# Optimization experiments

Measured on AMD Instinct MI355X. Metric: run time of the kernel, lower is better.

The kernel has to match this reference:

```python
import jax, jax.numpy as jnp
import numpy as np

DT = 0.01
V_REST = 0.0


def setup_inputs() -> dict:
    key = jax.random.key(0)
    ks = jax.random.split(key, 9)
    S, N, T = 64, 128, 1000
    w = jax.random.normal(ks[0], (N, N), dtype=jnp.float32) / jnp.sqrt(jnp.float32(N))
    ic = jax.random.uniform(ks[1], (N,), dtype=jnp.float32)
    v0 = jax.random.uniform(ks[2], (S, N), dtype=jnp.float32)
    i0 = jax.random.uniform(ks[3], (S, N), dtype=jnp.float32)
    # spike-clock state starts at minus an Exponential(1) draw; event fires when it hits 0
    u0 = jax.random.uniform(ks[4], (S, N), dtype=jnp.float32, minval=1e-6, maxval=1.0)
    s0 = jnp.log(u0)
    mu = jax.random.uniform(ks[5], (2,), dtype=jnp.float32, minval=0.5, maxval=1.0)
    sg = jax.random.normal(ks[6], (2, 2), dtype=jnp.float32)
    sigma = 0.1 * jnp.dot(sg, sg.T)  # PSD diffusion matrix as in __init__
    noise = jax.random.normal(ks[7], (T, S, N, 2), dtype=jnp.float32)
    ue = jax.random.uniform(ks[8], (T, S, N), dtype=jnp.float32, minval=1e-6, maxval=1.0)
    exp_draws = -jnp.log(ue)
    return {"w": w, "ic": ic, "v0": v0, "i0": i0, "s0": s0,
            "mu": mu, "sigma": sigma, "noise": noise, "exp_draws": exp_draws}


def reference(w, ic, v0, i0, s0, mu, sigma, noise, exp_draws):
    """Euler-Maruyama integration of the spiking-neuron jump-SDE.

    Per neuron state y = (v, i, s):
      dv = mu1*(i + ic - v) dt + (sigma dW)_0
      di = -mu2*i dt        + (sigma dW)_1
      ds = intensity_fn(v) dt   (intensity_fn = softplus)
    Spike event when s crosses 0 (cond_fn = y[:, 2]):
      v -> v_rest, postsynaptic currents i += spikes @ w, s -> -Exp(1) redraw.
    Returns ys of shape (samples, neurons, times, 3).
    """
    mu1, mu2 = mu[0], mu[1]
    dW = noise * jnp.sqrt(jnp.asarray(DT, noise.dtype))  # [T,S,N,2]

    def step(carry, xs):
        v, i, s = carry
        dw, edraw = xs
        # drift
        dv = mu1 * (i + ic - v)
        di = -mu2 * i
        ds = jax.nn.softplus(v)  # intensity_fn
        # diffusion on (v,i) channels: sigma @ dW per neuron
        nvi = jnp.einsum('snk,jk->snj', dw, sigma)  # [S,N,2]
        v = v + DT * dv + nvi[..., 0]
        i = i + DT * di + nvi[..., 1]
        s = s + DT * ds
        spike = s >= 0.0  # event detection (cond_fn hits zero)
        spk = spike.astype(v.dtype)
        i = i + spk @ w                    # network coupling jump
        v = jnp.where(spike, V_REST, v)    # membrane reset
        s = jnp.where(spike, -edraw, s)    # redraw exponential spike clock
        return (v, i, s), jnp.stack([v, i, s], axis=-1)  # [S,N,3]

    (_, _, _), ys = jax.lax.scan(step, (v0, i0, s0), (dW, exp_draws))
    # ys: [T,S,N,3] -> [S,N,T,3] (samples, neurons, times, 3)
    return jnp.transpose(ys, (1, 2, 0, 3))
```

## Files before the change

kernel.cpp:

```cpp
#include <hip/hip_runtime.h>
#include <cmath>

#define NS 64
#define NN 128
#define NT 1000
#define CH 8
#define WROWS 130
#define WL_DW (WROWS * NN)
#define OBUF_DW (2 * CH * 3 * NN)
#define LDS_BYTES ((WL_DW + OBUF_DW) * 4 + 32)

__device__ __forceinline__ float softplus_np(float x) {
    float r = fmaxf(x, 0.0f) + log1pf(expf(-fabsf(x)));
    return (x == 0.0f) ? 0.693147180559945309f : r;
}

__device__ __forceinline__ void sync_lds() {
    __builtin_amdgcn_sched_barrier(0);
    asm volatile("s_waitcnt lgkmcnt(0)" ::: "memory");
    __builtin_amdgcn_s_barrier();
    __builtin_amdgcn_sched_barrier(0);
}

__global__ __launch_bounds__(192) void snn_scan_kernel(
    const float* __restrict__ w,
    const float* __restrict__ ic,
    const float* __restrict__ v0,
    const float* __restrict__ i0,
    const float* __restrict__ s0,
    const float* __restrict__ mu,
    const float* __restrict__ sigma,
    const float* __restrict__ noise,
    const float* __restrict__ exp_draws,
    float* __restrict__ out)
{
    #pragma clang fp contract(off)
    extern __shared__ float smem[];
    float* wl   = smem;
    float* obuf = smem + WL_DW;
    unsigned long long* mslot =
        (unsigned long long*)(smem + WL_DW + OBUF_DW);

    const int samp = blockIdx.x;
    const int tid  = threadIdx.x;
    const int wid  = tid >> 6;
    const int l    = tid & 63;
    const int n    = (wid << 6) | l;

    if (tid < 128) {
        const float4* src = (const float4*)w;
        float4* dst = (float4*)wl;
        #pragma unroll
        for (int it = 0; it < 32; ++it)
            dst[it * 128 + tid] = src[it * 128 + tid];
        ((float2*)(wl + NN * NN))[tid] = make_float2(0.0f, 0.0f);
    }

    const float SQDT  = sqrtf(0.01f);
    const float DTf   = 0.01f;
    const float LOGE2 = 0.693147180559945309f;

    float* outb = out + (size_t)samp * NN * NT * 3;

    float mu1 = 0.f, negmu2 = 0.f, g00 = 0.f, g01 = 0.f, g10 = 0.f, g11 = 0.f;
    float icn = 0.f, v_ = 0.f, i_ = 0.f, s_ = 0.f, sp = 0.f;
    float2 nb0 = {}, nb1 = {}, nb2 = {}, nb3 = {}, nb4 = {}, nb5 = {}, nb6 = {}, nb7 = {};
    float  eb0 = 0, eb1 = 0, eb2 = 0, eb3 = 0, eb4 = 0, eb5 = 0, eb6 = 0, eb7 = 0;

    const float* nzb = noise + (size_t)samp * (NN * 2) + n * 2;
    const float* edb = exp_draws + (size_t)samp * NN + n;

    if (wid < 2) {
        __builtin_amdgcn_s_setprio(1);
        mu1 = mu[0]; negmu2 = -mu[1];
        g00 = sigma[0]; g01 = sigma[1]; g10 = sigma[2]; g11 = sigma[3];
        icn = ic[n];
        v_ = v0[samp * NN + n];
        i_ = i0[samp * NN + n];
        s_ = s0[samp * NN + n];
        sp = softplus_np(v_);
        nb0 = *(const float2*)(nzb + 0ull * (NS * NN * 2)); eb0 = edb[0ull * (NS * NN)];
        nb1 = *(const float2*)(nzb + 1ull * (NS * NN * 2)); eb1 = edb[1ull * (NS * NN)];
        nb2 = *(const float2*)(nzb + 2ull * (NS * NN * 2)); eb2 = edb[2ull * (NS * NN)];
        nb3 = *(const float2*)(nzb + 3ull * (NS * NN * 2)); eb3 = edb[3ull * (NS * NN)];
        nb4 = *(const float2*)(nzb + 4ull * (NS * NN * 2)); eb4 = edb[4ull * (NS * NN)];
        nb5 = *(const float2*)(nzb + 5ull * (NS * NN * 2)); eb5 = edb[5ull * (NS * NN)];
        nb6 = *(const float2*)(nzb + 6ull * (NS * NN * 2)); eb6 = edb[6ull * (NS * NN)];
        nb7 = *(const float2*)(nzb + 7ull * (NS * NN * 2)); eb7 = edb[7ull * (NS * NN)];
    }
    sync_lds();

    if (wid < 2) {
        int cur = 0;
        float* ob = obuf + n;

        auto STEP = [&](int k, int blk, float2& nb, float& eb) {
            #pragma clang fp contract(off)
            const int t = blk * CH + k;
            s_ = s_ + DTf * sp;
            const bool kk = (s_ >= 0.0f);
            const unsigned long long mym = __ballot(kk);
            if (l == 0) mslot[(k & 1) * 2 + wid] = mym;
            sync_lds();
            const float2 nz = nb;
            const float  ed = eb;
            const int tp = (t + 8) < NT ? (t + 8) : NT - 1;
            nb = *(const float2*)(nzb + (size_t)tp * (NS * NN * 2));
            eb = edb[(size_t)tp * (NS * NN)];

            const float dw0 = nz.x * SQDT, dw1 = nz.y * SQDT;
            const float nv = (dw0 * g00) + (dw1 * g01);
            const float ni = (dw0 * g10) + (dw1 * g11);
            const float tt = (i_ + icn) - v_;
            const float vt = (v_ + DTf * (mu1 * tt)) + nv;
            const float it = (i_ + DTf * (negmu2 * i_)) + ni;
            const float spv = softplus_np(vt);

            unsigned long long m0 = mslot[(k & 1) * 2 + 0];
            unsigned long long m1 = mslot[(k & 1) * 2 + 1];

            float a = 0.0f;
            if (m0 | m1) {
                auto ext1 = [&]() -> int {
                    const bool u0 = (m0 != 0);
                    const unsigned long long m = u0 ? m0 : m1;
                    const int b = m ? (int)__builtin_ctzll(m) : 99;
                    const int r = (b == 99) ? 128 : ((u0 ? 0 : 64) + b);
                    const unsigned long long m0n = m0 & (m0 - 1);
                    const unsigned long long m1n = m1 & (m1 - 1);
                    m0 = u0 ? m0n : m0;
                    m1 = u0 ? m1 : m1n;
                    return r;
                };
                const int r1 = ext1(); const int r2 = ext1();
                const int r3 = ext1(); const int r4 = ext1();
                const float q1 = wl[r1 * NN + n];
                const float q2 = wl[r2 * NN + n];
                const float q3 = wl[r3 * NN + n];
                const float q4 = wl[r4 * NN + n];
                a = q1;  a += q2;  a += q3;  a += q4;
                #pragma clang loop unroll(disable)
                while (m0 | m1) {
                    const int r = ext1();
                    a += wl[r * NN + n];
                }
            }
            i_ = it + a;

            v_ = kk ? 0.0f : vt;
            s_ = kk ? -ed : s_;
            sp = kk ? LOGE2 : spv;

            float* row = ob + (cur * CH * 3 + k * 3) * NN;
            row[0 * NN] = v_;
            row[1 * NN] = i_;
            row[2 * NN] = s_;
        };

        #pragma clang loop unroll(disable)
        for (int blk = 0; blk < NT / CH; ++blk) {
            STEP(0, blk, nb0, eb0);
            STEP(1, blk, nb1, eb1);
            STEP(2, blk, nb2, eb2);
            STEP(3, blk, nb3, eb3);
            STEP(4, blk, nb4, eb4);
            STEP(5, blk, nb5, eb5);
            STEP(6, blk, nb6, eb6);
            STEP(7, blk, nb7, eb7);
            cur ^= 1;
        }
    } else {
        auto flush3 = [&](int b, int tb0, int kk) {
            const float* ob2 = obuf + b * (CH * 3 * NN);
            #pragma unroll
            for (int j = 3 * kk; j < 3 * kk + 3; ++j) {
                const int f = j * 64 + l;
                const int nn2 = f / 12;
                const int da = 2 * (f - nn2 * 12);
                const float x = ob2[(da    ) * NN + nn2];
                const float y = ob2[(da + 1) * NN + nn2];
                *(float2*)(outb + (size_t)nn2 * (NT * 3) + (size_t)tb0 * 3 + da) =
                    make_float2(x, y);
            }
        };
        int cur = 0;
        #pragma clang loop unroll(disable)
        for (int blk = 0; blk < NT / CH; ++blk) {
            #pragma clang loop unroll(disable)
            for (int k = 0; k < CH; ++k) {
                sync_lds();
                if (blk > 0) flush3(cur ^ 1, (blk - 1) * CH, k);
            }
            cur ^= 1;
        }
    }

    sync_lds();

    if (wid == 2) {
        const float* ob2 = obuf + 0 * (CH * 3 * NN);
        #pragma unroll
        for (int j = 0; j < 24; ++j) {
            const int f = j * 64 + l;
            const int nn2 = f / 12;
            const int da = 2 * (f - nn2 * 12);
            const float x = ob2[(da    ) * NN + nn2];
            const float y = ob2[(da + 1) * NN + nn2];
            *(float2*)(outb + (size_t)nn2 * (NT * 3) + (size_t)(NT - CH) * 3 + da) =
                make_float2(x, y);
        }
    }
}

extern "C" void kernel_launch(void* const* d_in, const int* in_sizes, int n_in,
                              void* d_out, int out_size, void* d_ws, size_t ws_size,
                              hipStream_t stream) {
    const float* w         = (const float*)d_in[0];
    const float* ic        = (const float*)d_in[1];
    const float* v0        = (const float*)d_in[2];
    const float* i0        = (const float*)d_in[3];
    const float* s0        = (const float*)d_in[4];
    const float* mu        = (const float*)d_in[5];
    const float* sigma     = (const float*)d_in[6];
    const float* noise     = (const float*)d_in[7];
    const float* exp_draws = (const float*)d_in[8];
    float* out = (float*)d_out;

    (void)hipFuncSetAttribute((const void*)snn_scan_kernel,
                              hipFuncAttributeMaxDynamicSharedMemorySize,
                              LDS_BYTES);

    snn_scan_kernel<<<dim3(NS), dim3(192), LDS_BYTES, stream>>>(
        w, ic, v0, i0, s0, mu, sigma, noise, exp_draws, out);
}
```

Before: 575.4 us.

## Redundantly track mirror wave's spike clock to move barrier off critical path

Each compute wave now also integrates the spike clock of its partner neuron (n^64), so it can build both halves of the spike mask locally with two ballots instead of exchanging masks through LDS before the coupling step. The partner's softplus intensity is passed through a small LDS buffer after a barrier at the end of each step, one step delayed. This moves the barrier from the start of the step to the end, so the dependency chain into the weight-row gather is shorter. The output staging buffer is also padded to stride 129 to reduce bank conflicts. The cost is extra exp_draws loads, extra registers, and duplicated clock arithmetic.

```diff
diff --git a/kernel.cpp b/kernel.cpp
--- a/kernel.cpp
+++ b/kernel.cpp
@@ -5,10 +5,13 @@
 #define NN 128
 #define NT 1000
 #define CH 8
+#define NNP 129
 #define WROWS 130
 #define WL_DW (WROWS * NN)
-#define OBUF_DW (2 * CH * 3 * NN)
-#define LDS_BYTES ((WL_DW + OBUF_DW) * 4 + 32)
+#define OB_HALF (3 * CH * NNP)
+#define OBUF_DW (2 * OB_HALF)
+#define SPV_DW (2 * NN)
+#define LDS_BYTES ((WL_DW + OBUF_DW + SPV_DW) * 4)
 
 __device__ __forceinline__ float softplus_np(float x) {
     float r = fmaxf(x, 0.0f) + log1pf(expf(-fabsf(x)));
@@ -36,16 +39,16 @@
 {
     #pragma clang fp contract(off)
     extern __shared__ float smem[];
-    float* wl   = smem;
-    float* obuf = smem + WL_DW;
-    unsigned long long* mslot =
-        (unsigned long long*)(smem + WL_DW + OBUF_DW);
+    float* wl     = smem;
+    float* obuf   = smem + WL_DW;
+    float* spvbuf = smem + WL_DW + OBUF_DW;
 
     const int samp = blockIdx.x;
     const int tid  = threadIdx.x;
     const int wid  = tid >> 6;
     const int l    = tid & 63;
     const int n    = (wid << 6) | l;
+    const int nm   = n ^ 64;
 
     if (tid < 128) {
         const float4* src = (const float4*)w;
@@ -64,11 +67,15 @@
 
     float mu1 = 0.f, negmu2 = 0.f, g00 = 0.f, g01 = 0.f, g10 = 0.f, g11 = 0.f;
     float icn = 0.f, v_ = 0.f, i_ = 0.f, s_ = 0.f, sp = 0.f;
+    float s_m = 0.f, spvm_pend = 0.f;
+    bool  km_prev = false;
     float2 nb0 = {}, nb1 = {}, nb2 = {}, nb3 = {}, nb4 = {}, nb5 = {}, nb6 = {}, nb7 = {};
-    float  eb0 = 0, eb1 = 0, eb2 = 0, eb3 = 0, eb4 = 0, eb5 = 0, eb6 = 0, eb7 = 0;
+    float  eo0 = 0, eo1 = 0, eo2 = 0, eo3 = 0, eo4 = 0, eo5 = 0, eo6 = 0, eo7 = 0;
+    float  em0 = 0, em1 = 0, em2 = 0, em3 = 0, em4 = 0, em5 = 0, em6 = 0, em7 = 0;
 
     const float* nzb = noise + (size_t)samp * (NN * 2) + n * 2;
-    const float* edb = exp_draws + (size_t)samp * NN + n;
+    const float* edo = exp_draws + (size_t)samp * NN + n;
+    const float* edm = exp_draws + (size_t)samp * NN + nm;
 
     if (wid < 2) {
         __builtin_amdgcn_s_setprio(1);
@@ -79,35 +86,32 @@
         i_ = i0[samp * NN + n];
         s_ = s0[samp * NN + n];
         sp = softplus_np(v_);
-        nb0 = *(const float2*)(nzb + 0ull * (NS * NN * 2)); eb0 = edb[0ull * (NS * NN)];
-        nb1 = *(const float2*)(nzb + 1ull * (NS * NN * 2)); eb1 = edb[1ull * (NS * NN)];
-        nb2 = *(const float2*)(nzb + 2ull * (NS * NN * 2)); eb2 = edb[2ull * (NS * NN)];
-        nb3 = *(const float2*)(nzb + 3ull * (NS * NN * 2)); eb3 = edb[3ull * (NS * NN)];
-        nb4 = *(const float2*)(nzb + 4ull * (NS * NN * 2)); eb4 = edb[4ull * (NS * NN)];
-        nb5 = *(const float2*)(nzb + 5ull * (NS * NN * 2)); eb5 = edb[5ull * (NS * NN)];
-        nb6 = *(const float2*)(nzb + 6ull * (NS * NN * 2)); eb6 = edb[6ull * (NS * NN)];
-        nb7 = *(const float2*)(nzb + 7ull * (NS * NN * 2)); eb7 = edb[7ull * (NS * NN)];
+        s_m = s0[samp * NN + nm];
+        spvm_pend = softplus_np(v0[samp * NN + nm]);
+        nb0 = *(const float2*)(nzb + 0ull * (NS * NN * 2)); eo0 = edo[0ull * (NS * NN)]; em0 = edm[0ull * (NS * NN)];
+        nb1 = *(const float2*)(nzb + 1ull * (NS * NN * 2)); eo1 = edo[1ull * (NS * NN)]; em1 = edm[1ull * (NS * NN)];
+        nb2 = *(const float2*)(nzb + 2ull * (NS * NN * 2)); eo2 = edo[2ull * (NS * NN)]; em2 = edm[2ull * (NS * NN)];
+        nb3 = *(const float2*)(nzb + 3ull * (NS * NN * 2)); eo3 = edo[3ull * (NS * NN)]; em3 = edm[3ull * (NS * NN)];
+        nb4 = *(const float2*)(nzb + 4ull * (NS * NN * 2)); eo4 = edo[4ull * (NS * NN)]; em4 = edm[4ull * (NS * NN)];
+        nb5 = *(const float2*)(nzb + 5ull * (NS * NN * 2)); eo5 = edo[5ull * (NS * NN)]; em5 = edm[5ull * (NS * NN)];
+        nb6 = *(const float2*)(nzb + 6ull * (NS * NN * 2)); eo6 = edo[6ull * (NS * NN)]; em6 = edm[6ull * (NS * NN)];
+        nb7 = *(const float2*)(nzb + 7ull * (NS * NN * 2)); eo7 = edo[7ull * (NS * NN)]; em7 = edm[7ull * (NS * NN)];
     }
     sync_lds();
 
     if (wid < 2) {
-        int cur = 0;
-        float* ob = obuf + n;
-
-        auto STEP = [&](int k, int blk, float2& nb, float& eb) {
+        auto STEP = [&](int k, int blk, float2& nb, float& eo, float& em) {
             #pragma clang fp contract(off)
             const int t = blk * CH + k;
+            const int par = k & 1;
             s_ = s_ + DTf * sp;
             const bool kk = (s_ >= 0.0f);
-            const unsigned long long mym = __ballot(kk);
-            if (l == 0) mslot[(k & 1) * 2 + wid] = mym;
-            sync_lds();
-            const float2 nz = nb;
-            const float  ed = eb;
-            const int tp = (t + 8) < NT ? (t + 8) : NT - 1;
+            const unsigned long long mown = __ballot(kk);
+            const float2 nz = nb; const float edv = eo; const float edmv = em;
+            const int tp = (t + CH) < NT ? (t + CH) : NT - 1;
             nb = *(const float2*)(nzb + (size_t)tp * (NS * NN * 2));
-            eb = edb[(size_t)tp * (NS * NN)];
-
+            eo = edo[(size_t)tp * (NS * NN)];
+            em = edm[(size_t)tp * (NS * NN)];
             const float dw0 = nz.x * SQDT, dw1 = nz.y * SQDT;
             const float nv = (dw0 * g00) + (dw1 * g01);
             const float ni = (dw0 * g10) + (dw1 * g11);
@@ -115,10 +119,13 @@
             const float vt = (v_ + DTf * (mu1 * tt)) + nv;
             const float it = (i_ + DTf * (negmu2 * i_)) + ni;
             const float spv = softplus_np(vt);
-
-            unsigned long long m0 = mslot[(k & 1) * 2 + 0];
-            unsigned long long m1 = mslot[(k & 1) * 2 + 1];
-
+            spvbuf[par * NN + n] = spv;
+            const float spm = km_prev ? LOGE2 : spvm_pend;
+            s_m = s_m + DTf * spm;
+            const bool kmir = (s_m >= 0.0f);
+            const unsigned long long mmir = __ballot(kmir);
+            unsigned long long m0 = (wid == 0) ? mown : mmir;
+            unsigned long long m1 = (wid == 0) ? mmir : mown;
             float a = 0.0f;
             if (m0 | m1) {
                 auto ext1 = [&]() -> int {
@@ -146,66 +153,64 @@
                 }
             }
             i_ = it + a;
-
             v_ = kk ? 0.0f : vt;
-            s_ = kk ? -ed : s_;
+            s_ = kk ? -edv : s_;
             sp = kk ? LOGE2 : spv;
-
-            float* row = ob + (cur * CH * 3 + k * 3) * NN;
-            row[0 * NN] = v_;
-            row[1 * NN] = i_;
-            row[2 * NN] = s_;
+            s_m = kmir ? -edmv : s_m;
+            float* row = obuf + (blk & 1) * OB_HALF + (k * 3) * NNP + n;
+            row[0 * NNP] = v_;
+            row[1 * NNP] = i_;
+            row[2 * NNP] = s_;
+            sync_lds();
+            spvm_pend = spvbuf[par * NN + nm];
+            km_prev = kmir;
         };
 
         #pragma clang loop unroll(disable)
         for (int blk = 0; blk < NT / CH; ++blk) {
-            STEP(0, blk, nb0, eb0);
-            STEP(1, blk, nb1, eb1);
-            STEP(2, blk, nb2, eb2);
-            STEP(3, blk, nb3, eb3);
-            STEP(4, blk, nb4, eb4);
-            STEP(5, blk, nb5, eb5);
-            STEP(6, blk, nb6, eb6);
-            STEP(7, blk, nb7, eb7);
-            cur ^= 1;
+            STEP(0, blk, nb0, eo0, em0);
+            STEP(1, blk, nb1, eo1, em1);
+            STEP(2, blk, nb2, eo2, em2);
+            STEP(3, blk, nb3, eo3, em3);
+            STEP(4, blk, nb4, eo4, em4);
+            STEP(5, blk, nb5, eo5, em5);
+            STEP(6, blk, nb6, eo6, em6);
+            STEP(7, blk, nb7, eo7, em7);
         }
     } else {
-        auto flush3 = [&](int b, int tb0, int kk) {
-            const float* ob2 = obuf + b * (CH * 3 * NN);
+        auto flush3 = [&](int h, int tb0, int kk) {
+            const float* ob2 = obuf + h * OB_HALF;
             #pragma unroll
             for (int j = 3 * kk; j < 3 * kk + 3; ++j) {
                 const int f = j * 64 + l;
                 const int nn2 = f / 12;
                 const int da = 2 * (f - nn2 * 12);
-                const float x = ob2[(da    ) * NN + nn2];
-                const float y = ob2[(da + 1) * NN + nn2];
+                const float x = ob2[(da    ) * NNP + nn2];
+                const float y = ob2[(da + 1) * NNP + nn2];
                 *(float2*)(outb + (size_t)nn2 * (NT * 3) + (size_t)tb0 * 3 + da) =
                     make_float2(x, y);
             }
         };
-        int cur = 0;
         #pragma clang loop unroll(disable)
         for (int blk = 0; blk < NT / CH; ++blk) {
             #pragma clang loop unroll(disable)
             for (int k = 0; k < CH; ++k) {
                 sync_lds();
-                if (blk > 0) flush3(cur ^ 1, (blk - 1) * CH, k);
+                if (blk > 0) flush3((blk - 1) & 1, (blk - 1) * CH, k);
             }
-            cur ^= 1;
         }
     }
 
     sync_lds();
-
     if (wid == 2) {
-        const float* ob2 = obuf + 0 * (CH * 3 * NN);
+        const float* ob2 = obuf + ((NT / CH - 1) & 1) * OB_HALF;
         #pragma unroll
         for (int j = 0; j < 24; ++j) {
             const int f = j * 64 + l;
             const int nn2 = f / 12;
             const int da = 2 * (f - nn2 * 12);
-            const float x = ob2[(da    ) * NN + nn2];
-            const float y = ob2[(da + 1) * NN + nn2];
+            const float x = ob2[(da    ) * NNP + nn2];
+            const float y = ob2[(da + 1) * NNP + nn2];
             *(float2*)(outb + (size_t)nn2 * (NT * 3) + (size_t)(NT - CH) * 3 + da) =
                 make_float2(x, y);
         }
```

Result: no change. 583.9 us (+1.5%).

## Pack two samples per block sharing weight LDS, pad output buffer

Applied to the files above, without the earlier changes.

Each block now handles two samples with 384 threads (3 waves per sample), sharing one LDS copy of the weight matrix, and launches half as many blocks. The output staging buffer is padded to 129 columns to reduce LDS bank conflicts on the transposing flush, the sched_barriers and setprio are removed, and the unrolled spike gather is cut from 4 to 2 rows. The aim is to reduce per-block weight loading, improve the LDS read pattern, and shorten the common spike path. The cost is that both samples now synchronise on shared block-wide barriers, so each step waits on the slower of the two samples, and only 32 blocks run on a large GPU.

```diff
diff --git a/kernel.cpp b/kernel.cpp
--- a/kernel.cpp
+++ b/kernel.cpp
@@ -5,10 +5,13 @@
 #define NN 128
 #define NT 1000
 #define CH 8
+#define NNP 129
 #define WROWS 130
 #define WL_DW (WROWS * NN)
-#define OBUF_DW (2 * CH * 3 * NN)
-#define LDS_BYTES ((WL_DW + OBUF_DW) * 4 + 32)
+#define OB_HALF (3 * CH * NNP)
+#define OBUF_PS (2 * OB_HALF)
+#define MS_DW 8
+#define LDS_BYTES ((WL_DW + 2 * OBUF_PS + 2 * MS_DW) * 4)
 
 __device__ __forceinline__ float softplus_np(float x) {
     float r = fmaxf(x, 0.0f) + log1pf(expf(-fabsf(x)));
@@ -16,13 +19,12 @@
 }
 
 __device__ __forceinline__ void sync_lds() {
-    __builtin_amdgcn_sched_barrier(0);
     asm volatile("s_waitcnt lgkmcnt(0)" ::: "memory");
     __builtin_amdgcn_s_barrier();
-    __builtin_amdgcn_sched_barrier(0);
-}
-
-__global__ __launch_bounds__(192) void snn_scan_kernel(
+    asm volatile("" ::: "memory");
+}
+
+__global__ __launch_bounds__(384) void snn_scan_kernel(
     const float* __restrict__ w,
     const float* __restrict__ ic,
     const float* __restrict__ v0,
@@ -36,16 +38,19 @@
 {
     #pragma clang fp contract(off)
     extern __shared__ float smem[];
-    float* wl   = smem;
-    float* obuf = smem + WL_DW;
+    float* wl = smem;
+
+    const int tid = threadIdx.x;
+    const int wid = tid >> 6;
+    const int ss  = (wid >= 3) ? 1 : 0;
+    const int wr  = wid - 3 * ss;
+    const int l   = tid & 63;
+    const int samp = blockIdx.x * 2 + ss;
+    const int n    = (wr << 6) | l;
+
+    float* obuf = smem + WL_DW + ss * OBUF_PS;
     unsigned long long* mslot =
-        (unsigned long long*)(smem + WL_DW + OBUF_DW);
-
-    const int samp = blockIdx.x;
-    const int tid  = threadIdx.x;
-    const int wid  = tid >> 6;
-    const int l    = tid & 63;
-    const int n    = (wid << 6) | l;
+        (unsigned long long*)(smem + WL_DW + 2 * OBUF_PS) + ss * 4;
 
     if (tid < 128) {
         const float4* src = (const float4*)w;
@@ -70,8 +75,7 @@
     const float* nzb = noise + (size_t)samp * (NN * 2) + n * 2;
     const float* edb = exp_draws + (size_t)samp * NN + n;
 
-    if (wid < 2) {
-        __builtin_amdgcn_s_setprio(1);
+    if (wr < 2) {
         mu1 = mu[0]; negmu2 = -mu[1];
         g00 = sigma[0]; g01 = sigma[1]; g10 = sigma[2]; g11 = sigma[3];
         icn = ic[n];
@@ -90,21 +94,18 @@
     }
     sync_lds();
 
-    if (wid < 2) {
-        int cur = 0;
-        float* ob = obuf + n;
-
+    if (wr < 2) {
         auto STEP = [&](int k, int blk, float2& nb, float& eb) {
             #pragma clang fp contract(off)
             const int t = blk * CH + k;
             s_ = s_ + DTf * sp;
             const bool kk = (s_ >= 0.0f);
             const unsigned long long mym = __ballot(kk);
-            if (l == 0) mslot[(k & 1) * 2 + wid] = mym;
+            if (l == 0) mslot[(k & 1) * 2 + wr] = mym;
             sync_lds();
             const float2 nz = nb;
             const float  ed = eb;
-            const int tp = (t + 8) < NT ? (t + 8) : NT - 1;
+            const int tp = (t + CH) < NT ? (t + CH) : NT - 1;
             nb = *(const float2*)(nzb + (size_t)tp * (NS * NN * 2));
             eb = edb[(size_t)tp * (NS * NN)];
 
@@ -133,12 +134,9 @@
                     return r;
                 };
                 const int r1 = ext1(); const int r2 = ext1();
-                const int r3 = ext1(); const int r4 = ext1();
                 const float q1 = wl[r1 * NN + n];
                 const float q2 = wl[r2 * NN + n];
-                const float q3 = wl[r3 * NN + n];
-                const float q4 = wl[r4 * NN + n];
-                a = q1;  a += q2;  a += q3;  a += q4;
+                a = q1;  a += q2;
                 #pragma clang loop unroll(disable)
                 while (m0 | m1) {
                     const int r = ext1();
@@ -151,10 +149,10 @@
             s_ = kk ? -ed : s_;
             sp = kk ? LOGE2 : spv;
 
-            float* row = ob + (cur * CH * 3 + k * 3) * NN;
-            row[0 * NN] = v_;
-            row[1 * NN] = i_;
-            row[2 * NN] = s_;
+            float* row = obuf + (blk & 1) * OB_HALF + (k * 3) * NNP + n;
+            row[0 * NNP] = v_;
+            row[1 * NNP] = i_;
+            row[2 * NNP] = s_;
         };
 
         #pragma clang loop unroll(disable)
@@ -167,45 +165,41 @@
             STEP(5, blk, nb5, eb5);
             STEP(6, blk, nb6, eb6);
             STEP(7, blk, nb7, eb7);
-            cur ^= 1;
         }
     } else {
-        auto flush3 = [&](int b, int tb0, int kk) {
-            const float* ob2 = obuf + b * (CH * 3 * NN);
+        auto flush3 = [&](int h, int tb0, int kk) {
+            const float* ob2 = obuf + h * OB_HALF;
             #pragma unroll
             for (int j = 3 * kk; j < 3 * kk + 3; ++j) {
                 const int f = j * 64 + l;
                 const int nn2 = f / 12;
                 const int da = 2 * (f - nn2 * 12);
-                const float x = ob2[(da    ) * NN + nn2];
-                const float y = ob2[(da + 1) * NN + nn2];
+                const float x = ob2[(da    ) * NNP + nn2];
+                const float y = ob2[(da + 1) * NNP + nn2];
                 *(float2*)(outb + (size_t)nn2 * (NT * 3) + (size_t)tb0 * 3 + da) =
                     make_float2(x, y);
             }
         };
-        int cur = 0;
         #pragma clang loop unroll(disable)
         for (int blk = 0; blk < NT / CH; ++blk) {
             #pragma clang loop unroll(disable)
             for (int k = 0; k < CH; ++k) {
                 sync_lds();
-                if (blk > 0) flush3(cur ^ 1, (blk - 1) * CH, k);
+                if (blk > 0) flush3((blk - 1) & 1, (blk - 1) * CH, k);
             }
-            cur ^= 1;
         }
     }
 
     sync_lds();
-
-    if (wid == 2) {
-        const float* ob2 = obuf + 0 * (CH * 3 * NN);
+    if (wr == 2) {
+        const float* ob2 = obuf + ((NT / CH - 1) & 1) * OB_HALF;
         #pragma unroll
         for (int j = 0; j < 24; ++j) {
             const int f = j * 64 + l;
             const int nn2 = f / 12;
             const int da = 2 * (f - nn2 * 12);
-            const float x = ob2[(da    ) * NN + nn2];
-            const float y = ob2[(da + 1) * NN + nn2];
+            const float x = ob2[(da    ) * NNP + nn2];
+            const float y = ob2[(da + 1) * NNP + nn2];
             *(float2*)(outb + (size_t)nn2 * (NT * 3) + (size_t)(NT - CH) * 3 + da) =
                 make_float2(x, y);
         }
@@ -230,6 +224,6 @@
                               hipFuncAttributeMaxDynamicSharedMemorySize,
                               LDS_BYTES);
 
-    snn_scan_kernel<<<dim3(NS), dim3(192), LDS_BYTES, stream>>>(
+    snn_scan_kernel<<<dim3(NS / 2), dim3(384), LDS_BYTES, stream>>>(
         w, ic, v0, i0, s0, mu, sigma, noise, exp_draws, out);
 }
```

After: 715.8 us. +24.4%, slower.

## Compute all 128 neurons in one wavefront to remove per-step barriers

Applied to the files above, without the earlier changes.

The scan now runs in a single wave, with each lane handling two neurons as float2 pairs. Spike masks come from two ballots inside the wave, so the per-timestep LDS mask exchange and block barrier go away, leaving one barrier per 8-step chunk. The weight matrix is re-laid out as interleaved pairs, and the output staging buffer is padded to avoid bank conflicts. The trade-off is less parallelism on the serial critical path: each lane now does twice the softplus and gather work, and a single writer wave flushes a whole chunk at a time.

```diff
diff --git a/kernel.cpp b/kernel.cpp
--- a/kernel.cpp
+++ b/kernel.cpp
@@ -5,10 +5,15 @@
 #define NN 128
 #define NT 1000
 #define CH 8
+#define OBP 65
 #define WROWS 130
-#define WL_DW (WROWS * NN)
-#define OBUF_DW (2 * CH * 3 * NN)
-#define LDS_BYTES ((WL_DW + OBUF_DW) * 4 + 32)
+#define WP_F2 (WROWS * 64)
+#define WL_DW (WP_F2 * 2)
+#define OB_HALF_F2 (CH * 3 * OBP)
+#define OBUF_DW (2 * OB_HALF_F2 * 2)
+#define LDS_BYTES ((WL_DW + OBUF_DW) * 4)
+
+typedef float f2 __attribute__((ext_vector_type(2)));
 
 __device__ __forceinline__ float softplus_np(float x) {
     float r = fmaxf(x, 0.0f) + log1pf(expf(-fabsf(x)));
@@ -16,13 +21,12 @@
 }
 
 __device__ __forceinline__ void sync_lds() {
-    __builtin_amdgcn_sched_barrier(0);
     asm volatile("s_waitcnt lgkmcnt(0)" ::: "memory");
     __builtin_amdgcn_s_barrier();
-    __builtin_amdgcn_sched_barrier(0);
-}
-
-__global__ __launch_bounds__(192) void snn_scan_kernel(
+    asm volatile("" ::: "memory");
+}
+
+__global__ __launch_bounds__(128) void snn_scan_kernel(
     const float* __restrict__ w,
     const float* __restrict__ ic,
     const float* __restrict__ v0,
@@ -36,179 +40,166 @@
 {
     #pragma clang fp contract(off)
     extern __shared__ float smem[];
-    float* wl   = smem;
-    float* obuf = smem + WL_DW;
-    unsigned long long* mslot =
-        (unsigned long long*)(smem + WL_DW + OBUF_DW);
+    f2* wp2   = (f2*)smem;
+    f2* obuf2 = (f2*)(smem + WL_DW);
 
     const int samp = blockIdx.x;
     const int tid  = threadIdx.x;
     const int wid  = tid >> 6;
     const int l    = tid & 63;
-    const int n    = (wid << 6) | l;
-
-    if (tid < 128) {
-        const float4* src = (const float4*)w;
-        float4* dst = (float4*)wl;
+
+    {
         #pragma unroll
-        for (int it = 0; it < 32; ++it)
-            dst[it * 128 + tid] = src[it * 128 + tid];
-        ((float2*)(wl + NN * NN))[tid] = make_float2(0.0f, 0.0f);
+        for (int j = 0; j < 64; ++j) {
+            const int p = j * 128 + tid;
+            const int r = p >> 6, c = p & 63;
+            wp2[p] = (f2){w[r * 128 + c], w[r * 128 + 64 + c]};
+        }
+        wp2[8192 + tid] = (f2){0.0f, 0.0f};
     }
 
-    const float SQDT  = sqrtf(0.01f);
-    const float DTf   = 0.01f;
+    const f2 SQ  = (f2)(sqrtf(0.01f));
+    const f2 DTv = (f2)(0.01f);
     const float LOGE2 = 0.693147180559945309f;
 
     float* outb = out + (size_t)samp * NN * NT * 3;
 
-    float mu1 = 0.f, negmu2 = 0.f, g00 = 0.f, g01 = 0.f, g10 = 0.f, g11 = 0.f;
-    float icn = 0.f, v_ = 0.f, i_ = 0.f, s_ = 0.f, sp = 0.f;
-    float2 nb0 = {}, nb1 = {}, nb2 = {}, nb3 = {}, nb4 = {}, nb5 = {}, nb6 = {}, nb7 = {};
-    float  eb0 = 0, eb1 = 0, eb2 = 0, eb3 = 0, eb4 = 0, eb5 = 0, eb6 = 0, eb7 = 0;
-
-    const float* nzb = noise + (size_t)samp * (NN * 2) + n * 2;
-    const float* edb = exp_draws + (size_t)samp * NN + n;
-
-    if (wid < 2) {
-        __builtin_amdgcn_s_setprio(1);
-        mu1 = mu[0]; negmu2 = -mu[1];
-        g00 = sigma[0]; g01 = sigma[1]; g10 = sigma[2]; g11 = sigma[3];
-        icn = ic[n];
-        v_ = v0[samp * NN + n];
-        i_ = i0[samp * NN + n];
-        s_ = s0[samp * NN + n];
-        sp = softplus_np(v_);
-        nb0 = *(const float2*)(nzb + 0ull * (NS * NN * 2)); eb0 = edb[0ull * (NS * NN)];
-        nb1 = *(const float2*)(nzb + 1ull * (NS * NN * 2)); eb1 = edb[1ull * (NS * NN)];
-        nb2 = *(const float2*)(nzb + 2ull * (NS * NN * 2)); eb2 = edb[2ull * (NS * NN)];
-        nb3 = *(const float2*)(nzb + 3ull * (NS * NN * 2)); eb3 = edb[3ull * (NS * NN)];
-        nb4 = *(const float2*)(nzb + 4ull * (NS * NN * 2)); eb4 = edb[4ull * (NS * NN)];
-        nb5 = *(const float2*)(nzb + 5ull * (NS * NN * 2)); eb5 = edb[5ull * (NS * NN)];
-        nb6 = *(const float2*)(nzb + 6ull * (NS * NN * 2)); eb6 = edb[6ull * (NS * NN)];
-        nb7 = *(const float2*)(nzb + 7ull * (NS * NN * 2)); eb7 = edb[7ull * (NS * NN)];
+    f2 mu1v = 0.f, nm2v = 0.f, g00v = 0.f, g01v = 0.f, g10v = 0.f, g11v = 0.f;
+    f2 icv = 0.f, v = 0.f, i = 0.f, s = 0.f, sp = 0.f;
+    f2 pA0 = 0.f, pA1 = 0.f, pA2 = 0.f, pA3 = 0.f;
+    f2 pB0 = 0.f, pB1 = 0.f, pB2 = 0.f, pB3 = 0.f;
+    f2 e0 = 0.f, e1 = 0.f, e2 = 0.f, e3 = 0.f;
+
+    const float* nzb = noise + (size_t)samp * (NN * 2) + l * 2;
+    const float* edb = exp_draws + (size_t)samp * NN + l;
+
+    if (wid == 0) {
+        mu1v = (f2)(mu[0]); nm2v = (f2)(-mu[1]);
+        g00v = (f2)(sigma[0]); g01v = (f2)(sigma[1]);
+        g10v = (f2)(sigma[2]); g11v = (f2)(sigma[3]);
+        icv = (f2){ic[l], ic[l + 64]};
+        v = (f2){v0[samp * NN + l], v0[samp * NN + l + 64]};
+        i = (f2){i0[samp * NN + l], i0[samp * NN + l + 64]};
+        s = (f2){s0[samp * NN + l], s0[samp * NN + l + 64]};
+        sp = (f2){softplus_np(v.x), softplus_np(v.y)};
+        pA0 = *(const f2*)(nzb + 0ull * (NS * NN * 2));
+        pB0 = *(const f2*)(nzb + 0ull * (NS * NN * 2) + 128);
+        e0  = (f2){edb[0ull * (NS * NN)], edb[0ull * (NS * NN) + 64]};
+        pA1 = *(const f2*)(nzb + 1ull * (NS * NN * 2));
+        pB1 = *(const f2*)(nzb + 1ull * (NS * NN * 2) + 128);
+        e1  = (f2){edb[1ull * (NS * NN)], edb[1ull * (NS * NN) + 64]};
+        pA2 = *(const f2*)(nzb + 2ull * (NS * NN * 2));
+        pB2 = *(const f2*)(nzb + 2ull * (NS * NN * 2) + 128);
+        e2  = (f2){edb[2ull * (NS * NN)], edb[2ull * (NS * NN) + 64]};
+        pA3 = *(const f2*)(nzb + 3ull * (NS * NN * 2));
+        pB3 = *(const f2*)(nzb + 3ull * (NS * NN * 2) + 128);
+        e3  = (f2){edb[3ull * (NS * NN)], edb[3ull * (NS * NN) + 64]};
     }
     sync_lds();
 
-    if (wid < 2) {
-        int cur = 0;
-        float* ob = obuf + n;
-
-        auto STEP = [&](int k, int blk, float2& nb, float& eb) {
+    if (wid == 0) {
+        auto pf = [&](f2& pA, f2& pB, f2& e, int tt) {
+            const int tc = tt < NT ? tt : NT - 1;
+            const float* pn = nzb + (size_t)tc * (NS * NN * 2);
+            const float* pe = edb + (size_t)tc * (NS * NN);
+            pA = *(const f2*)(pn);
+            pB = *(const f2*)(pn + 128);
+            e  = (f2){pe[0], pe[64]};
+        };
+
+        auto step = [&](int tm, int h, const f2 pA, const f2 pB, const f2 e) {
             #pragma clang fp contract(off)
-            const int t = blk * CH + k;
-            s_ = s_ + DTf * sp;
-            const bool kk = (s_ >= 0.0f);
-            const unsigned long long mym = __ballot(kk);
-            if (l == 0) mslot[(k & 1) * 2 + wid] = mym;
-            sync_lds();
-            const float2 nz = nb;
-            const float  ed = eb;
-            const int tp = (t + 8) < NT ? (t + 8) : NT - 1;
-            nb = *(const float2*)(nzb + (size_t)tp * (NS * NN * 2));
-            eb = edb[(size_t)tp * (NS * NN)];
-
-            const float dw0 = nz.x * SQDT, dw1 = nz.y * SQDT;
-            const float nv = (dw0 * g00) + (dw1 * g01);
-            const float ni = (dw0 * g10) + (dw1 * g11);
-            const float tt = (i_ + icn) - v_;
-            const float vt = (v_ + DTf * (mu1 * tt)) + nv;
-            const float it = (i_ + DTf * (negmu2 * i_)) + ni;
-            const float spv = softplus_np(vt);
-
-            unsigned long long m0 = mslot[(k & 1) * 2 + 0];
-            unsigned long long m1 = mslot[(k & 1) * 2 + 1];
-
-            float a = 0.0f;
+            const f2 px = (f2){pA.x, pB.x};
+            const f2 py = (f2){pA.y, pB.y};
+            const f2 dw0 = px * SQ;
+            const f2 dw1 = py * SQ;
+            const f2 nv = (dw0 * g00v) + (dw1 * g01v);
+            const f2 ni = (dw0 * g10v) + (dw1 * g11v);
+            const f2 tt = (i + icv) - v;
+            const f2 vt = (v + DTv * (mu1v * tt)) + nv;
+            const f2 it = (i + DTv * (nm2v * i)) + ni;
+            s = s + DTv * sp;
+
+            const bool k0 = (s.x >= 0.0f), k1 = (s.y >= 0.0f);
+            unsigned long long m0 = __ballot(k0);
+            unsigned long long m1 = __ballot(k1);
+
+            const f2 spv = (f2){softplus_np(vt.x), softplus_np(vt.y)};
+
+            f2 a = (f2){0.0f, 0.0f};
             if (m0 | m1) {
                 auto ext1 = [&]() -> int {
                     const bool u0 = (m0 != 0);
                     const unsigned long long m = u0 ? m0 : m1;
                     const int b = m ? (int)__builtin_ctzll(m) : 99;
-                    const int r = (b == 99) ? 128 : ((u0 ? 0 : 64) + b);
+                    const int r = (b == 99) ? 128 : (u0 ? b : 64 + b);
                     const unsigned long long m0n = m0 & (m0 - 1);
                     const unsigned long long m1n = m1 & (m1 - 1);
                     m0 = u0 ? m0n : m0;
                     m1 = u0 ? m1 : m1n;
                     return r;
                 };
-                const int r1 = ext1(); const int r2 = ext1();
-                const int r3 = ext1(); const int r4 = ext1();
-                const float q1 = wl[r1 * NN + n];
-                const float q2 = wl[r2 * NN + n];
-                const float q3 = wl[r3 * NN + n];
-                const float q4 = wl[r4 * NN + n];
-                a = q1;  a += q2;  a += q3;  a += q4;
+                const int r1 = ext1();
+                const int r2 = ext1();
+                const f2 q1 = wp2[r1 * 64 + l];
+                const f2 q2 = wp2[r2 * 64 + l];
+                a = q1;
+                a += q2;
                 #pragma clang loop unroll(disable)
                 while (m0 | m1) {
                     const int r = ext1();
-                    a += wl[r * NN + n];
+                    a += wp2[r * 64 + l];
                 }
             }
-            i_ = it + a;
-
-            v_ = kk ? 0.0f : vt;
-            s_ = kk ? -ed : s_;
-            sp = kk ? LOGE2 : spv;
-
-            float* row = ob + (cur * CH * 3 + k * 3) * NN;
-            row[0 * NN] = v_;
-            row[1 * NN] = i_;
-            row[2 * NN] = s_;
+            i = it + a;
+
+            v.x = k0 ? 0.0f : vt.x;       v.y = k1 ? 0.0f : vt.y;
+            s.x = k0 ? -e.x : s.x;        s.y = k1 ? -e.y : s.y;
+            sp.x = k0 ? LOGE2 : spv.x;    sp.y = k1 ? LOGE2 : spv.y;
+
+            f2* ob2 = obuf2 + h * OB_HALF_F2 + (tm * 3) * OBP + l;
+            ob2[0 * OBP] = v;
+            ob2[1 * OBP] = i;
+            ob2[2 * OBP] = s;
         };
 
         #pragma clang loop unroll(disable)
         for (int blk = 0; blk < NT / CH; ++blk) {
-            STEP(0, blk, nb0, eb0);
-            STEP(1, blk, nb1, eb1);
-            STEP(2, blk, nb2, eb2);
-            STEP(3, blk, nb3, eb3);
-            STEP(4, blk, nb4, eb4);
-            STEP(5, blk, nb5, eb5);
-            STEP(6, blk, nb6, eb6);
-            STEP(7, blk, nb7, eb7);
-            cur ^= 1;
+            const int t = blk * CH, h = blk & 1;
+            step(0, h, pA0, pB0, e0); pf(pA0, pB0, e0, t + 4);
+            step(1, h, pA1, pB1, e1); pf(pA1, pB1, e1, t + 5);
+            step(2, h, pA2, pB2, e2); pf(pA2, pB2, e2, t + 6);
+            step(3, h, pA3, pB3, e3); pf(pA3, pB3, e3, t + 7);
+            step(4, h, pA0, pB0, e0); pf(pA0, pB0, e0, t + 8);
+            step(5, h, pA1, pB1, e1); pf(pA1, pB1, e1, t + 9);
+            step(6, h, pA2, pB2, e2); pf(pA2, pB2, e2, t + 10);
+            step(7, h, pA3, pB3, e3); pf(pA3, pB3, e3, t + 11);
+            sync_lds();
         }
     } else {
-        auto flush3 = [&](int b, int tb0, int kk) {
-            const float* ob2 = obuf + b * (CH * 3 * NN);
+        auto flushHalf = [&](int h, int tb0) {
+            const float* ob = (const float*)(obuf2 + h * OB_HALF_F2);
             #pragma unroll
-            for (int j = 3 * kk; j < 3 * kk + 3; ++j) {
+            for (int j = 0; j < 24; ++j) {
                 const int f = j * 64 + l;
-                const int nn2 = f / 12;
-                const int da = 2 * (f - nn2 * 12);
-                const float x = ob2[(da    ) * NN + nn2];
-                const float y = ob2[(da + 1) * NN + nn2];
-                *(float2*)(outb + (size_t)nn2 * (NT * 3) + (size_t)tb0 * 3 + da) =
+                const int n = f / 12;
+                const int rr = f - n * 12;
+                const int da = 2 * rr;
+                const int ka = da / 3, ca = da - ka * 3;
+                const int kb = (da + 1) / 3, cb = (da + 1) - kb * 3;
+                const int col = (n & 63) * 2 + (n >> 6);
+                const float x = ob[((ka * 3 + ca) * OBP) * 2 + col];
+                const float y = ob[((kb * 3 + cb) * OBP) * 2 + col];
+                *(float2*)(outb + (size_t)n * (NT * 3) + (size_t)tb0 * 3 + da) =
                     make_float2(x, y);
             }
         };
-        int cur = 0;
         #pragma clang loop unroll(disable)
         for (int blk = 0; blk < NT / CH; ++blk) {
-            #pragma clang loop unroll(disable)
-            for (int k = 0; k < CH; ++k) {
-                sync_lds();
-                if (blk > 0) flush3(cur ^ 1, (blk - 1) * CH, k);
-            }
-            cur ^= 1;
+            if (blk > 0) flushHalf((blk - 1) & 1, (blk - 1) * CH);
+            sync_lds();
         }
-    }
-
-    sync_lds();
-
-    if (wid == 2) {
-        const float* ob2 = obuf + 0 * (CH * 3 * NN);
-        #pragma unroll
-        for (int j = 0; j < 24; ++j) {
-            const int f = j * 64 + l;
-            const int nn2 = f / 12;
-            const int da = 2 * (f - nn2 * 12);
-            const float x = ob2[(da    ) * NN + nn2];
-            const float y = ob2[(da + 1) * NN + nn2];
-            *(float2*)(outb + (size_t)nn2 * (NT * 3) + (size_t)(NT - CH) * 3 + da) =
-                make_float2(x, y);
-        }
+        flushHalf((NT / CH - 1) & 1, NT - CH);
     }
 }
 
@@ -230,6 +221,6 @@
                               hipFuncAttributeMaxDynamicSharedMemorySize,
                               LDS_BYTES);
 
-    snn_scan_kernel<<<dim3(NS), dim3(192), LDS_BYTES, stream>>>(
+    snn_scan_kernel<<<dim3(NS), dim3(128), LDS_BYTES, stream>>>(
         w, ic, v0, i0, s0, mu, sigma, noise, exp_draws, out);
 }
```

Result: slower. 674.0 us (+17.1%).
